# Optimization experiments

Hardware: AMD Instinct MI355X
Metric: run time of the kernel (lower is better)

Reference implementation:

```python
import jax, jax.numpy as jnp
import numpy as np

B, S, E, H = 2, 2048, 2048, 16
D = E // H  # head_dim = 128
EPS = 1e-5


def setup_inputs() -> dict:
    key = jax.random.key(0)
    ks = jax.random.split(key, 16)
    s_e = 1.0 / np.sqrt(E)
    s_f = 1.0 / np.sqrt(4 * E)
    return {
        "x": jax.random.normal(ks[0], (B, S, E), jnp.float32),
        "ln1_w": jnp.ones((E,), jnp.float32) + 0.01 * jax.random.normal(ks[1], (E,)),
        "ln1_b": 0.01 * jax.random.normal(ks[2], (E,)),
        "wq": s_e * jax.random.normal(ks[3], (E, E), jnp.float32),
        "wk": s_e * jax.random.normal(ks[4], (E, E), jnp.float32),
        "wv": s_e * jax.random.normal(ks[5], (E, E), jnp.float32),
        "wo": s_e * jax.random.normal(ks[6], (E, E), jnp.float32),
        "bo": 0.01 * jax.random.normal(ks[7], (E,)),
        "ln2_w": jnp.ones((E,), jnp.float32) + 0.01 * jax.random.normal(ks[8], (E,)),
        "ln2_b": 0.01 * jax.random.normal(ks[9], (E,)),
        "w1": s_e * jax.random.normal(ks[10], (E, 4 * E), jnp.float32),
        "b1": 0.01 * jax.random.normal(ks[11], (4 * E,)),
        "w2": s_f * jax.random.normal(ks[12], (4 * E, E), jnp.float32),
        "b2": 0.01 * jax.random.normal(ks[13], (E,)),
    }


def _layernorm(x, w, b):
    mu = jnp.mean(x, axis=-1, keepdims=True)
    var = jnp.var(x, axis=-1, keepdims=True)
    return (x - mu) * jax.lax.rsqrt(var + EPS) * w + b


def _attention(x, wq, wk, wv, wo, bo):
    # x: [B,S,E] -> q,k,v: [B,H,S,D]
    def split(t):
        return t.reshape(B, S, H, D).transpose(0, 2, 1, 3)
    q = split(x @ wq)
    k = split(x @ wk)
    v = split(x @ wv)
    scores = jnp.einsum("bhqd,bhkd->bhqk", q, k)  # [B,H,S,S]
    causal = jnp.triu(jnp.ones((S, S), bool), k=1)
    scores = jnp.where(causal, -jnp.inf, scores)
    # NOTE: faithful to source -- scaling applied after masking, inside softmax arg
    attn = jax.nn.softmax(scores / np.sqrt(D), axis=-1)
    ctx = jnp.einsum("bhqk,bhkd->bhqd", attn, v)
    ctx = ctx.transpose(0, 2, 1, 3).reshape(B, S, E)
    return ctx @ wo + bo


def reference(x, ln1_w, ln1_b, wq, wk, wv, wo, bo, ln2_w, ln2_b, w1, b1, w2, b2):
    shortcut = x
    x1 = _layernorm(x, ln1_w, ln1_b)
    attn_out = _attention(x1, wq, wk, wv, wo, bo)
    a = attn_out + shortcut
    # NOTE: faithful to source quirk -- second shortcut is post-LN1 x1, not a
    y = _layernorm(a, ln2_w, ln2_b)
    y = jax.nn.gelu(y @ w1 + b1, approximate=False) @ w2 + b2
    return x1 + y
```

## Files before the change

### kernel.cpp

```cpp
#include <hip/hip_runtime.h>
#include <math.h>

typedef unsigned short u16;
typedef unsigned int u32;
typedef __attribute__((ext_vector_type(8))) short short8;
typedef __attribute__((ext_vector_type(4))) float f32x4;
typedef __attribute__((ext_vector_type(16))) float f32x16;
typedef __attribute__((ext_vector_type(4))) u32 u32x4;
typedef __attribute__((ext_vector_type(2))) u32 u32x2;

#define DEVFN static __device__ __forceinline__

DEVFN u16 f2bf(float x) {
  union { float f; u32 u; } v; v.f = x;
  u32 r = v.u + 0x7fffu + ((v.u >> 16) & 1u);
  return (u16)(r >> 16);
}
DEVFN float bf2f(u16 h) {
  union { u32 u; float f; } v; v.u = ((u32)h) << 16;
  return v.f;
}
DEVFN u32 packbf2(float a, float b) {
  return (u32)f2bf(a) | ((u32)f2bf(b) << 16);
}
DEVFN void gl2lds16(const u16* g, u16* l) {
  __builtin_amdgcn_global_load_lds(
      (const __attribute__((address_space(1))) u32*)g,
      (__attribute__((address_space(3))) u32*)l, 16, 0, 0);
}
DEVFN float gelu_exact(float v) {
  float s = v * 0.70710678118654752f;
  float ax = fabsf(s);
  float t = __builtin_amdgcn_rcpf(1.0f + 0.3275911f * ax);
  float poly = t * (0.254829592f +
               t * (-0.284496736f +
               t * (1.421413741f +
               t * (-1.453152027f + t * 1.061405429f))));
  float e = __expf(-s * s);
  float er = 1.0f - poly * e;
  er = (s < 0.f) ? -er : er;
  return 0.5f * v * (1.0f + er);
}

#define VMW8() asm volatile("s_waitcnt vmcnt(8)" ::: "memory")
#define VMW6() asm volatile("s_waitcnt vmcnt(6)" ::: "memory")
#define VMW2() asm volatile("s_waitcnt vmcnt(2)" ::: "memory")
#define VMW0() asm volatile("s_waitcnt vmcnt(0)" ::: "memory")
#define LGKM0() asm volatile("s_waitcnt lgkmcnt(0)" ::: "memory")
#define CFENCE() asm volatile("" ::: "memory")
#define BARRIER() do { CFENCE(); __builtin_amdgcn_s_barrier(); CFENCE(); } while (0)

__global__ __launch_bounds__(256) void tconv_k(const float* __restrict__ in,
                                               u16* __restrict__ out, int K, int N) {
  __shared__ float tile[32][33];
  int n0 = blockIdx.x << 5, k0 = blockIdx.y << 5;
  int tx = threadIdx.x & 31, ty = threadIdx.x >> 5;
#pragma unroll
  for (int i = 0; i < 32; i += 8)
    tile[ty + i][tx] = in[(long)(k0 + ty + i) * N + n0 + tx];
  __syncthreads();
#pragma unroll
  for (int i = 0; i < 32; i += 8)
    out[(long)(n0 + ty + i) * K + k0 + tx] = f2bf(tile[tx][ty + i]);
}

__global__ __launch_bounds__(256) void ln1_k(const float* __restrict__ x,
                                             const float* __restrict__ w,
                                             const float* __restrict__ b,
                                             float* __restrict__ y32,
                                             u16* __restrict__ y16) {
  long base = (long)blockIdx.x * 2048;
  int t = threadIdx.x;
  float4 v0 = ((const float4*)(x + base))[2 * t];
  float4 v1 = ((const float4*)(x + base))[2 * t + 1];
  float xv[8];
  *(float4*)xv = v0; *(float4*)(xv + 4) = v1;
  float s = 0.f, ss = 0.f;
#pragma unroll
  for (int i = 0; i < 8; ++i) { s += xv[i]; ss += xv[i] * xv[i]; }
#pragma unroll
  for (int m = 1; m < 64; m <<= 1) { s += __shfl_xor(s, m); ss += __shfl_xor(ss, m); }
  __shared__ float rs[4], rss[4];
  int wave = t >> 6;
  if ((t & 63) == 0) { rs[wave] = s; rss[wave] = ss; }
  __syncthreads();
  s = rs[0] + rs[1] + rs[2] + rs[3];
  ss = rss[0] + rss[1] + rss[2] + rss[3];
  float mean = s * (1.f / 2048.f);
  float var = ss * (1.f / 2048.f) - mean * mean;
  float inv = rsqrtf(var + 1e-5f);
  float wv[8], bv[8];
  *(float4*)wv = ((const float4*)w)[2 * t]; *(float4*)(wv + 4) = ((const float4*)w)[2 * t + 1];
  *(float4*)bv = ((const float4*)b)[2 * t]; *(float4*)(bv + 4) = ((const float4*)b)[2 * t + 1];
  float yv[8];
#pragma unroll
  for (int i = 0; i < 8; ++i) yv[i] = (xv[i] - mean) * inv * wv[i] + bv[i];
  ((float4*)(y32 + base))[2 * t] = *(float4*)yv;
  ((float4*)(y32 + base))[2 * t + 1] = *(float4*)(yv + 4);
  u32x4 ov;
#pragma unroll
  for (int i = 0; i < 4; ++i) ov[i] = packbf2(yv[2 * i], yv[2 * i + 1]);
  ((u32x4*)(y16 + base))[t] = ov;
}

__global__ __launch_bounds__(256) void ln2_k(const u16* __restrict__ a,
                                             const float* __restrict__ w,
                                             const float* __restrict__ b,
                                             u16* __restrict__ y) {
  long base = (long)blockIdx.x * 2048;
  int t = threadIdx.x;
  u32x4 pv = ((const u32x4*)(a + base))[t];
  float xv[8];
#pragma unroll
  for (int i = 0; i < 4; ++i) {
    xv[2 * i] = bf2f((u16)(pv[i] & 0xffffu));
    xv[2 * i + 1] = bf2f((u16)(pv[i] >> 16));
  }
  float s = 0.f, ss = 0.f;
#pragma unroll
  for (int i = 0; i < 8; ++i) { s += xv[i]; ss += xv[i] * xv[i]; }
#pragma unroll
  for (int m = 1; m < 64; m <<= 1) { s += __shfl_xor(s, m); ss += __shfl_xor(ss, m); }
  __shared__ float rs[4], rss[4];
  int wave = t >> 6;
  if ((t & 63) == 0) { rs[wave] = s; rss[wave] = ss; }
  __syncthreads();
  s = rs[0] + rs[1] + rs[2] + rs[3];
  ss = rss[0] + rss[1] + rss[2] + rss[3];
  float mean = s * (1.f / 2048.f);
  float var = ss * (1.f / 2048.f) - mean * mean;
  float inv = rsqrtf(var + 1e-5f);
  float wv[8], bv[8];
  *(float4*)wv = ((const float4*)w)[2 * t]; *(float4*)(wv + 4) = ((const float4*)w)[2 * t + 1];
  *(float4*)bv = ((const float4*)b)[2 * t]; *(float4*)(bv + 4) = ((const float4*)b)[2 * t + 1];
  u32x4 ov;
#pragma unroll
  for (int i = 0; i < 4; ++i) {
    float y0 = (xv[2 * i] - mean) * inv * wv[2 * i] + bv[2 * i];
    float y1 = (xv[2 * i + 1] - mean) * inv * wv[2 * i + 1] + bv[2 * i + 1];
    ov[i] = packbf2(y0, y1);
  }
  ((u32x4*)(y + base))[t] = ov;
}

template <int MODE>
__global__ __launch_bounds__(512, 2) void gemm2x_k(const u16* __restrict__ A,
                                                   const u16* __restrict__ W,
                                                   void* __restrict__ outp,
                                                   const float* __restrict__ bias) {
  constexpr int nM = 16;
  constexpr int nN = (MODE == 0) ? 24 : (MODE == 3) ? 32 : 8;
  constexpr int KS = (MODE == 5) ? 2 : 1;
  constexpr int KK = (MODE == 5) ? 4096 : 2048;
  constexpr long LD = (MODE == 5) ? 8192 : 2048;
  constexpr int nt = KK / 64;
  constexpr int nwg = nM * nN * KS;
  __shared__ __align__(16) u16 lds[2][32768];
  const int t = threadIdx.x, lane = t & 63, wave = t >> 6;
  const int g = lane >> 4, r16 = lane & 15;
  const int wm = wave >> 2, wn = wave & 3;
  const int orig = blockIdx.y * gridDim.x + blockIdx.x;
  const int sw = (orig & 7) * (nwg >> 3) + (orig >> 3);
  const int mi = sw % nM;
  const int rest = sw / nM;
  const int ni = (MODE == 5) ? (rest & 7) : rest;
  const int ks = (MODE == 5) ? (rest >> 3) : 0;
  const long m0 = (long)mi * 256, n0 = (long)ni * 256;
  const long k0 = (long)ks * 4096;
  const int rl = lane >> 3, cl = lane & 7;

  auto stA = [&](int b, int half, int tile) {
#pragma unroll
    for (int q = 0; q < 2; ++q) {
      int rr = (wave * 2 + q) * 8 + rl;
      gl2lds16(A + (m0 + half * 128 + rr) * LD + k0 + (long)tile * 64 + (cl ^ (rr & 7)) * 8,
               &lds[b][half * 8192 + (wave * 2 + q) * 512]);
    }
  };
  auto stB = [&](int b, int half, int tile) {
#pragma unroll
    for (int q = 0; q < 2; ++q) {
      int rr = (wave * 2 + q) * 8 + rl;
      gl2lds16(W + (n0 + half * 128 + rr) * LD + k0 + (long)tile * 64 + (cl ^ (rr & 7)) * 8,
               &lds[b][16384 + half * 8192 + (wave * 2 + q) * 512]);
    }
  };

  f32x4 acc[8][4] = {};
  stA(0, 0, 0); stA(0, 1, 0); stB(0, 0, 0); stB(0, 1, 0);
  stA(1, 0, 1); stA(1, 1, 1); stB(1, 0, 1); stB(1, 1, 1);

  for (int tt = 0; tt < nt; ++tt) {
    const int cur = tt & 1;
    const u16* Lc = &lds[cur][0];
    VMW8();
    BARRIER();
    short8 a0[8], b0[4];
#pragma unroll
    for (int ii = 0; ii < 8; ++ii) {
      int row = wm * 128 + ii * 16 + r16;
      a0[ii] = *(const short8*)(Lc + row * 64 + (g ^ (row & 7)) * 8);
    }
#pragma unroll
    for (int jj = 0; jj < 4; ++jj) {
      int row = wn * 64 + jj * 16 + r16;
      b0[jj] = *(const short8*)(Lc + 16384 + row * 64 + (g ^ (row & 7)) * 8);
    }
    __builtin_amdgcn_s_setprio(1);
#pragma unroll
    for (int ii = 0; ii < 8; ++ii)
#pragma unroll
      for (int jj = 0; jj < 4; ++jj)
        acc[ii][jj] = __builtin_amdgcn_mfma_f32_16x16x32_bf16(a0[ii], b0[jj], acc[ii][jj], 0, 0, 0);
    __builtin_amdgcn_s_setprio(0);
    short8 a1[8], b1f[4];
#pragma unroll
    for (int ii = 0; ii < 8; ++ii) {
      int row = wm * 128 + ii * 16 + r16;
      a1[ii] = *(const short8*)(Lc + row * 64 + ((4 | g) ^ (row & 7)) * 8);
    }
#pragma unroll
    for (int jj = 0; jj < 4; ++jj) {
      int row = wn * 64 + jj * 16 + r16;
      b1f[jj] = *(const short8*)(Lc + 16384 + row * 64 + ((4 | g) ^ (row & 7)) * 8);
    }
    LGKM0();
    BARRIER();
    {
      const int ts = (tt + 2 < nt) ? tt + 2 : nt - 1;
      stA(cur, 0, ts); stA(cur, 1, ts); stB(cur, 0, ts); stB(cur, 1, ts);
    }
    __builtin_amdgcn_s_setprio(1);
#pragma unroll
    for (int ii = 0; ii < 8; ++ii)
#pragma unroll
      for (int jj = 0; jj < 4; ++jj)
        acc[ii][jj] = __builtin_amdgcn_mfma_f32_16x16x32_bf16(a1[ii], b1f[jj], acc[ii][jj], 0, 0, 0);
    __builtin_amdgcn_s_setprio(0);
  }
  VMW0();

#pragma unroll
  for (int ii = 0; ii < 8; ++ii) {
#pragma unroll
    for (int jj = 0; jj < 4; ++jj) {
#pragma unroll
      for (int r = 0; r < 4; ++r) {
        long mg = m0 + wm * 128 + ii * 16 + g * 4 + r;
        long ng = n0 + wn * 64 + jj * 16 + r16;
        float v = acc[ii][jj][r];
        if constexpr (MODE == 0) {
          long which = ng >> 11;
          long nloc = ng & 2047;
          long bb = mg >> 11, sq = mg & 2047;
          long hh = nloc >> 7, dd = nloc & 127;
          long idx = (which < 2) ? (((bb * 16 + hh) * 2048 + sq) * 128 + dd)
                                 : (((bb * 16 + hh) * 128 + dd) * 2048 + sq);
          ((u16*)outp)[which * 8388608 + idx] = f2bf(v);
        } else if constexpr (MODE == 3) {
          v = gelu_exact(v + bias[ng]);
          ((u16*)outp)[mg * 8192 + ng] = f2bf(v);
        } else {
          ((float*)outp)[(long)ks * 8388608 + mg * 2048 + ng] = v;
        }
      }
    }
  }
}

__global__ __launch_bounds__(256) void red_k(const float* __restrict__ p,
                                             const float* __restrict__ bias,
                                             const float* __restrict__ resid,
                                             float* __restrict__ out) {
  long i = (long)blockIdx.x * 256 + threadIdx.x;
  for (long idx = i; idx < 2097152; idx += 2048 * 256) {
    float4 a = ((const float4*)p)[idx];
    float4 b = ((const float4*)(p + 8388608))[idx];
    float4 r = ((const float4*)resid)[idx];
    float4 bs = ((const float4*)bias)[idx & 511];
    float4 o;
    o.x = a.x + b.x + r.x + bs.x;
    o.y = a.y + b.y + r.y + bs.y;
    o.z = a.z + b.z + r.z + bs.z;
    o.w = a.w + b.w + r.w + bs.w;
    ((float4*)out)[idx] = o;
  }
}

template <int MODE>
__global__ __launch_bounds__(512, 2) void gemm3_k(const u16* __restrict__ A,
                                                  const u16* __restrict__ W,
                                                  void* __restrict__ outp,
                                                  const float* __restrict__ bias,
                                                  const float* __restrict__ resid,
                                                  int M, int N, int K) {
  __shared__ __align__(16) u16 lds[3][24576];
  const int t = threadIdx.x, lane = t & 63, wave = t >> 6;
  const int g = lane >> 4, r16 = lane & 15;
  const int wm = wave >> 2, wn = wave & 3;
  const int nM = M >> 7;
  const int nwg = gridDim.x * gridDim.y;
  const int orig = blockIdx.y * gridDim.x + blockIdx.x;
  const int sw = (nwg & 7) ? orig : ((orig & 7) * (nwg >> 3) + (orig >> 3));
  const long m0 = (long)(sw % nM) * 128, n0 = (long)(sw / nM) * 256;
  const int nt = K >> 6;
  const long Kl = K;
  const int rl = lane >> 3, cc = lane & 7;

  auto stA = [&](u16* Lb, long tile) {
#pragma unroll
    for (int q = 0; q < 2; ++q) {
      int rr = (wave * 2 + q) * 8 + rl;
      int c = cc ^ (rr & 7);
      gl2lds16(A + (m0 + rr) * Kl + (tile << 6) + c * 8, Lb + (wave * 2 + q) * 512);
    }
  };
  auto stB = [&](u16* Lb, int half, long tile) {
#pragma unroll
    for (int q = 0; q < 2; ++q) {
      int rr = (wave * 2 + q) * 8 + rl;
      int c = cc ^ (rr & 7);
      gl2lds16(W + (n0 + half * 128 + rr) * Kl + (tile << 6) + c * 8,
               Lb + 8192 + half * 8192 + (wave * 2 + q) * 512);
    }
  };

  f32x4 acc[4][4] = {};
  u16* L0 = &lds[0][0];
  u16* L1 = &lds[1][0];
  u16* L2 = &lds[2][0];

  stA(L0, 0); stB(L0, 0, 0); stB(L0, 1, 0);
  if (nt > 1) { stA(L1, 1); stB(L1, 0, 1); stB(L1, 1, 1); }
  if (nt > 2) { VMW6(); } else { VMW0(); }
  BARRIER();

  for (int tt = 0; tt < nt; ++tt) {
    const long ts = (tt + 2 < nt) ? (long)(tt + 2) : (long)(nt - 1);
    short8 af[4][2], bf[2][2];
#pragma unroll
    for (int ii2 = 0; ii2 < 4; ++ii2) {
      int row = (ii2 * 2 + wm) * 16 + r16;
#pragma unroll
      for (int kk = 0; kk < 2; ++kk)
        af[ii2][kk] = *(const short8*)(L0 + row * 64 + (((kk << 2) | g) ^ (row & 7)) * 8);
    }
#pragma unroll
    for (int jj2 = 0; jj2 < 2; ++jj2) {
      int row = (jj2 * 4 + wn) * 16 + r16;
#pragma unroll
      for (int kk = 0; kk < 2; ++kk)
        bf[jj2][kk] = *(const short8*)(L0 + 8192 + row * 64 + (((kk << 2) | g) ^ (row & 7)) * 8);
    }
    stA(L2, ts); stB(L2, 0, ts);
    __builtin_amdgcn_s_setprio(1);
#pragma unroll
    for (int ii2 = 0; ii2 < 4; ++ii2)
#pragma unroll
      for (int jj2 = 0; jj2 < 2; ++jj2)
#pragma unroll
        for (int kk = 0; kk < 2; ++kk)
          acc[ii2][jj2] = __builtin_amdgcn_mfma_f32_16x16x32_bf16(
              af[ii2][kk], bf[jj2][kk], acc[ii2][jj2], 0, 0, 0);
    __builtin_amdgcn_s_setprio(0);
    BARRIER();
#pragma unroll
    for (int jj2 = 0; jj2 < 2; ++jj2) {
      int row = ((2 + jj2) * 4 + wn) * 16 + r16;
#pragma unroll
      for (int kk = 0; kk < 2; ++kk)
        bf[jj2][kk] = *(const short8*)(L0 + 8192 + row * 64 + (((kk << 2) | g) ^ (row & 7)) * 8);
    }
    stB(L2, 1, ts);
    __builtin_amdgcn_s_setprio(1);
#pragma unroll
    for (int ii2 = 0; ii2 < 4; ++ii2)
#pragma unroll
      for (int jj2 = 0; jj2 < 2; ++jj2)
#pragma unroll
        for (int kk = 0; kk < 2; ++kk)
          acc[ii2][2 + jj2] = __builtin_amdgcn_mfma_f32_16x16x32_bf16(
              af[ii2][kk], bf[jj2][kk], acc[ii2][2 + jj2], 0, 0, 0);
    __builtin_amdgcn_s_setprio(0);
    VMW6(); BARRIER();
    u16* tmp = L0; L0 = L1; L1 = L2; L2 = tmp;
  }
  VMW0();

  const long Nl = N;
#pragma unroll
  for (int ii = 0; ii < 4; ++ii) {
#pragma unroll
    for (int jj = 0; jj < 4; ++jj) {
#pragma unroll
      for (int r = 0; r < 4; ++r) {
        long mg = m0 + (ii * 2 + wm) * 16 + g * 4 + r;
        long ng = n0 + (jj * 4 + wn) * 16 + r16;
        float v = acc[ii][jj][r];
        if constexpr (MODE == 2) {
          v += bias[ng] + resid[mg * Nl + ng];
          ((u16*)outp)[mg * Nl + ng] = f2bf(v);
        } else {
          v += bias[ng] + resid[mg * Nl + ng];
          ((float*)outp)[mg * Nl + ng] = v;
        }
      }
    }
  }
}

__global__ __launch_bounds__(256, 2) void attn2_k(const u16* __restrict__ Qp,
                                                  const u16* __restrict__ Kp,
                                                  const u16* __restrict__ Vp,
                                                  u16* __restrict__ ctx) {
  __shared__ __align__(16) u16 KsL[2][64 * 128];
  __shared__ __align__(16) u16 VsL[2][128 * 64];
  const int qt = gridDim.x - 1 - blockIdx.x;
  const int bh = blockIdx.y;
  const int t = threadIdx.x, lane = t & 63, wave = t >> 6;
  const int l31 = lane & 31, hi = lane >> 5;
  const int q0 = qt * 128, qw0 = q0 + wave * 32;
  const int qg = qw0 + l31;
  const u16* Qh = Qp + (long)bh * 2048 * 128;
  const u16* Kh = Kp + (long)bh * 2048 * 128;
  const u16* Vh = Vp + (long)bh * 128 * 2048;
  const int nkt = qt * 2 + 2;
  const int ktmax = (qw0 + 31) >> 6;
  const float cs = 0.12753042923810058f;

  short8 qf[8];
#pragma unroll
  for (int ds = 0; ds < 8; ++ds)
    qf[ds] = *(const short8*)(Qh + (long)qg * 128 + ds * 16 + hi * 8);

  f32x16 O0 = {}, O1 = {}, O2 = {}, O3 = {};
  float m = -INFINITY, l = 0.f;

  auto stage = [&](int b, int kt) {
#pragma unroll
    for (int q = 0; q < 4; ++q) {
      int r = wave * 16 + q * 4 + (lane >> 4);
      int c = (lane & 15) ^ (r & 15);
      gl2lds16(Kh + ((long)kt * 64 + r) * 128 + c * 8,
               &KsL[b][(wave * 16 + q * 4) * 128]);
    }
#pragma unroll
    for (int q = 0; q < 4; ++q) {
      int r = wave * 32 + q * 8 + (lane >> 3);
      int c = (lane & 7) ^ (r & 7);
      gl2lds16(Vh + (long)r * 2048 + kt * 64 + c * 8,
               &VsL[b][(wave * 32 + q * 8) * 64]);
    }
  };

  stage(0, 0);
  VMW0(); BARRIER();

  for (int kt = 0; kt < nkt; ++kt) {
    const int cur = kt & 1;
    if (kt + 1 < nkt) stage(cur ^ 1, kt + 1);
    if (kt <= ktmax) {
      f32x16 S0 = {}, S1 = {};
      __builtin_amdgcn_s_setprio(1);
#pragma unroll
      for (int ds = 0; ds < 8; ++ds) {
        int c0 = ((ds * 2 + hi) ^ (l31 & 15)) * 8;
        short8 k0 = *(const short8*)(&KsL[cur][l31 * 128 + c0]);
        int r1 = 32 + l31;
        int c1 = ((ds * 2 + hi) ^ (r1 & 15)) * 8;
        short8 k1 = *(const short8*)(&KsL[cur][r1 * 128 + c1]);
        S0 = __builtin_amdgcn_mfma_f32_32x32x16_bf16(k0, qf[ds], S0, 0, 0, 0);
        S1 = __builtin_amdgcn_mfma_f32_32x32x16_bf16(k1, qf[ds], S1, 0, 0, 0);
      }
      __builtin_amdgcn_s_setprio(0);
      float p[32];
#pragma unroll
      for (int i = 0; i < 16; ++i) { p[i] = S0[i]; p[16 + i] = S1[i]; }
      if (kt * 64 + 63 > qw0) {
#pragma unroll
        for (int ks = 0; ks < 2; ++ks)
#pragma unroll
          for (int r = 0; r < 16; ++r) {
            int kg = kt * 64 + ks * 32 + (r & 3) + 8 * (r >> 2) + 4 * hi;
            if (kg > qg) p[ks * 16 + r] = -INFINITY;
          }
      }
      float tmax = p[0];
#pragma unroll
      for (int i = 1; i < 32; ++i) tmax = fmaxf(tmax, p[i]);
      tmax = fmaxf(tmax, __shfl_xor(tmax, 32));
      float mnew = fmaxf(m, tmax);
      float corr = __builtin_amdgcn_exp2f((m - mnew) * cs);
      float ls = 0.f;
#pragma unroll
      for (int i = 0; i < 32; ++i) {
        p[i] = __builtin_amdgcn_exp2f((p[i] - mnew) * cs);
        ls += p[i];
      }
      ls += __shfl_xor(ls, 32);
      l = l * corr + ls;
      m = mnew;
#pragma unroll
      for (int i = 0; i < 16; ++i) {
        O0[i] *= corr; O1[i] *= corr; O2[i] *= corr; O3[i] *= corr;
      }
      short8 pf[4];
#pragma unroll
      for (int gg = 0; gg < 4; ++gg) {
        u32 u_, v_, w_, z_;
        asm("v_cvt_pk_bf16_f32 %0, %1, %2" : "=v"(u_) : "v"(p[gg * 8 + 0]), "v"(p[gg * 8 + 1]));
        asm("v_cvt_pk_bf16_f32 %0, %1, %2" : "=v"(v_) : "v"(p[gg * 8 + 2]), "v"(p[gg * 8 + 3]));
        asm("v_cvt_pk_bf16_f32 %0, %1, %2" : "=v"(w_) : "v"(p[gg * 8 + 4]), "v"(p[gg * 8 + 5]));
        asm("v_cvt_pk_bf16_f32 %0, %1, %2" : "=v"(z_) : "v"(p[gg * 8 + 6]), "v"(p[gg * 8 + 7]));
        asm("v_permlane32_swap_b32 %0, %1" : "+v"(u_), "+v"(w_));
        asm("v_permlane32_swap_b32 %0, %1" : "+v"(v_), "+v"(z_));
        union { u32 w4[4]; short8 s; } cv;
        cv.w4[0] = u_; cv.w4[1] = v_; cv.w4[2] = w_; cv.w4[3] = z_;
        pf[gg] = cv.s;
      }
      __builtin_amdgcn_s_setprio(1);
#define PVROW(ds, OO)                                                          \
  {                                                                            \
    int row = (ds)*32 + l31;                                                   \
    _Pragma("unroll") for (int gg = 0; gg < 4; ++gg) {                         \
      short8 vf = *(const short8*)(&VsL[cur][row * 64 +                        \
                                             (((gg * 2 + hi) ^ (row & 7)) * 8)]); \
      OO = __builtin_amdgcn_mfma_f32_32x32x16_bf16(vf, pf[gg], OO, 0, 0, 0);   \
    }                                                                          \
  }
      PVROW(0, O0); PVROW(1, O1); PVROW(2, O2); PVROW(3, O3);
#undef PVROW
      __builtin_amdgcn_s_setprio(0);
    }
    VMW0(); BARRIER();
  }

  const float inv = 1.f / l;
  u16* cp = ctx + ((long)(bh >> 4) * 2048 + qg) * 2048 + (bh & 15) * 128;
#define WROUT(OO, dsb)                                                         \
  _Pragma("unroll") for (int rg = 0; rg < 4; ++rg) {                           \
    int d = (dsb)*32 + 8 * rg + 4 * hi;                                        \
    u32x2 wv;                                                                  \
    wv[0] = packbf2(OO[4 * rg] * inv, OO[4 * rg + 1] * inv);                   \
    wv[1] = packbf2(OO[4 * rg + 2] * inv, OO[4 * rg + 3] * inv);               \
    *(u32x2*)(cp + d) = wv;                                                    \
  }
  WROUT(O0, 0); WROUT(O1, 1); WROUT(O2, 2); WROUT(O3, 3);
#undef WROUT
}

extern "C" void kernel_launch(void* const* d_in, const int* in_sizes, int n_in,
                              void* d_out, int out_size, void* d_ws, size_t ws_size,
                              hipStream_t stream) {
  const float* x = (const float*)d_in[0];
  const float* ln1w = (const float*)d_in[1];
  const float* ln1b = (const float*)d_in[2];
  const float* wq = (const float*)d_in[3];
  const float* wk = (const float*)d_in[4];
  const float* wv = (const float*)d_in[5];
  const float* wo = (const float*)d_in[6];
  const float* bo = (const float*)d_in[7];
  const float* ln2w = (const float*)d_in[8];
  const float* ln2b = (const float*)d_in[9];
  const float* w1 = (const float*)d_in[10];
  const float* b1 = (const float*)d_in[11];
  const float* w2 = (const float*)d_in[12];
  const float* b2 = (const float*)d_in[13];
  float* out = (float*)d_out;
  char* ws = (char*)d_ws;

  float* x1f = (float*)(ws + 0);
  u16* x1b = (u16*)(ws + 33554432);
  u16* wqt = (u16*)(ws + 50331648);
  u16* wkt = (u16*)(ws + 58720256);
  u16* wvt = (u16*)(ws + 67108864);
  u16* wot = (u16*)(ws + 75497472);
  u16* w1t = (u16*)(ws + 83886080);
  u16* w2t = (u16*)(ws + 117440512);
  u16* qb = (u16*)(ws + 150994944);
  u16* kb = (u16*)(ws + 167772160);
  u16* vb = (u16*)(ws + 184549376);
  u16* ctxb = (u16*)(ws + 201326592);
  u16* ab = (u16*)(ws + 218103808);
  u16* y0b = (u16*)(ws + 234881024);
  u16* hb = qb;
  float* pbuf = (float*)(ws + 50331648);

  tconv_k<<<dim3(64, 64), 256, 0, stream>>>(wq, wqt, 2048, 2048);
  tconv_k<<<dim3(64, 64), 256, 0, stream>>>(wk, wkt, 2048, 2048);
  tconv_k<<<dim3(64, 64), 256, 0, stream>>>(wv, wvt, 2048, 2048);
  tconv_k<<<dim3(64, 64), 256, 0, stream>>>(wo, wot, 2048, 2048);
  tconv_k<<<dim3(256, 64), 256, 0, stream>>>(w1, w1t, 2048, 8192);
  tconv_k<<<dim3(64, 256), 256, 0, stream>>>(w2, w2t, 8192, 2048);
  ln1_k<<<4096, 256, 0, stream>>>(x, ln1w, ln1b, x1f, x1b);
  gemm2x_k<0><<<dim3(16, 24), 512, 0, stream>>>(x1b, wqt, qb, nullptr);
  attn2_k<<<dim3(16, 32), 256, 0, stream>>>(qb, kb, vb, ctxb);
  gemm3_k<2><<<dim3(32, 8), 512, 0, stream>>>(ctxb, wot, ab, bo, x, 4096, 2048, 2048);
  ln2_k<<<4096, 256, 0, stream>>>(ab, ln2w, ln2b, y0b);
  gemm2x_k<3><<<dim3(16, 32), 512, 0, stream>>>(y0b, w1t, hb, b1);
  gemm2x_k<5><<<dim3(16, 16), 512, 0, stream>>>(hb, w2t, pbuf, nullptr);
  red_k<<<2048, 256, 0, stream>>>(pbuf, b2, x1f, out);
}
```

Measured before the change: 644.0 us.

## Restructure big GEMM main loop into four-phase quadrant ping-pong schedule

The 256x256 GEMM main loop is reorganised into four quadrant phases (A-low/B-low, A-low/B-high, A-high/B-low, A-high/B-high). Each phase uses both k-halves, and the global-to-LDS loads for the next tile are spread between the phases with barriers in between. The LDS staging layout is rearranged so each quarter-tile can be refilled once its readers are finished. The goal is to interleave LDS reads, global prefetch and MFMA work more finely, in the style of an 8-wave ping-pong. Launch bounds drop to one block per CU, and the extra barriers add synchronisation cost.

```diff
diff --git a/kernel.cpp b/kernel.cpp
--- a/kernel.cpp
+++ b/kernel.cpp
@@ -44,7 +44,6 @@
 
 #define VMW8() asm volatile("s_waitcnt vmcnt(8)" ::: "memory")
 #define VMW6() asm volatile("s_waitcnt vmcnt(6)" ::: "memory")
-#define VMW2() asm volatile("s_waitcnt vmcnt(2)" ::: "memory")
 #define VMW0() asm volatile("s_waitcnt vmcnt(0)" ::: "memory")
 #define LGKM0() asm volatile("s_waitcnt lgkmcnt(0)" ::: "memory")
 #define CFENCE() asm volatile("" ::: "memory")
@@ -144,7 +143,7 @@
 }
 
 template <int MODE>
-__global__ __launch_bounds__(512, 2) void gemm2x_k(const u16* __restrict__ A,
+__global__ __launch_bounds__(512, 1) void gemm8p_k(const u16* __restrict__ A,
                                                    const u16* __restrict__ W,
                                                    void* __restrict__ outp,
                                                    const float* __restrict__ bias) {
@@ -169,74 +168,116 @@
   const long k0 = (long)ks * 4096;
   const int rl = lane >> 3, cl = lane & 7;
 
-  auto stA = [&](int b, int half, int tile) {
+  auto stAq = [&](int b, int grp, int ts) {
 #pragma unroll
     for (int q = 0; q < 2; ++q) {
-      int rr = (wave * 2 + q) * 8 + rl;
-      gl2lds16(A + (m0 + half * 128 + rr) * LD + k0 + (long)tile * 64 + (cl ^ (rr & 7)) * 8,
-               &lds[b][half * 8192 + (wave * 2 + q) * 512]);
+      int rb = q * 128 + grp * 64 + wave * 8;
+      int rr = rb + rl;
+      gl2lds16(A + (m0 + rr) * LD + k0 + (long)ts * 64 + (cl ^ (rr & 7)) * 8,
+               &lds[b][rb * 64]);
     }
   };
-  auto stB = [&](int b, int half, int tile) {
+  auto stBq = [&](int b, int grp, int ts) {
 #pragma unroll
     for (int q = 0; q < 2; ++q) {
-      int rr = (wave * 2 + q) * 8 + rl;
-      gl2lds16(W + (n0 + half * 128 + rr) * LD + k0 + (long)tile * 64 + (cl ^ (rr & 7)) * 8,
-               &lds[b][16384 + half * 8192 + (wave * 2 + q) * 512]);
+      int rb = q * 128 + (wave >> 2) * 64 + (wave & 3) * 8 + grp * 32;
+      int rr = rb + rl;
+      gl2lds16(W + (n0 + rr) * LD + k0 + (long)ts * 64 + (cl ^ (rr & 7)) * 8,
+               &lds[b][16384 + rb * 64]);
     }
   };
 
   f32x4 acc[8][4] = {};
-  stA(0, 0, 0); stA(0, 1, 0); stB(0, 0, 0); stB(0, 1, 0);
-  stA(1, 0, 1); stA(1, 1, 1); stB(1, 0, 1); stB(1, 1, 1);
+  short8 afl[4][2], afh[4][2], bfl[2][2], bfh[2][2];
+
+  stAq(0, 0, 0); stBq(0, 0, 0); stAq(0, 1, 0); stBq(0, 1, 0);
+  stAq(1, 0, 1); stBq(1, 0, 1); stAq(1, 1, 1); stBq(1, 1, 1);
+  VMW8();
+  BARRIER();
 
   for (int tt = 0; tt < nt; ++tt) {
     const int cur = tt & 1;
     const u16* Lc = &lds[cur][0];
-    VMW8();
+    const int ts = (tt + 2 < nt) ? tt + 2 : nt - 1;
+#pragma unroll
+    for (int ii = 0; ii < 4; ++ii) {
+      int row = wm * 128 + ii * 16 + r16;
+#pragma unroll
+      for (int kk = 0; kk < 2; ++kk)
+        afl[ii][kk] = *(const short8*)(Lc + row * 64 + (((kk << 2) | g) ^ (row & 7)) * 8);
+    }
+#pragma unroll
+    for (int jj = 0; jj < 2; ++jj) {
+      int row = wn * 64 + jj * 16 + r16;
+#pragma unroll
+      for (int kk = 0; kk < 2; ++kk)
+        bfl[jj][kk] = *(const short8*)(Lc + 16384 + row * 64 + (((kk << 2) | g) ^ (row & 7)) * 8);
+    }
+    BARRIER(); LGKM0();
+    __builtin_amdgcn_s_setprio(1);
+#pragma unroll
+    for (int ii = 0; ii < 4; ++ii)
+#pragma unroll
+      for (int jj = 0; jj < 2; ++jj)
+#pragma unroll
+        for (int kk = 0; kk < 2; ++kk)
+          acc[ii][jj] = __builtin_amdgcn_mfma_f32_16x16x32_bf16(
+              afl[ii][kk], bfl[jj][kk], acc[ii][jj], 0, 0, 0);
+    __builtin_amdgcn_s_setprio(0);
     BARRIER();
-    short8 a0[8], b0[4];
-#pragma unroll
-    for (int ii = 0; ii < 8; ++ii) {
-      int row = wm * 128 + ii * 16 + r16;
-      a0[ii] = *(const short8*)(Lc + row * 64 + (g ^ (row & 7)) * 8);
-    }
-#pragma unroll
-    for (int jj = 0; jj < 4; ++jj) {
-      int row = wn * 64 + jj * 16 + r16;
-      b0[jj] = *(const short8*)(Lc + 16384 + row * 64 + (g ^ (row & 7)) * 8);
-    }
+#pragma unroll
+    for (int jj = 0; jj < 2; ++jj) {
+      int row = wn * 64 + 32 + jj * 16 + r16;
+#pragma unroll
+      for (int kk = 0; kk < 2; ++kk)
+        bfh[jj][kk] = *(const short8*)(Lc + 16384 + row * 64 + (((kk << 2) | g) ^ (row & 7)) * 8);
+    }
+    stAq(cur, 0, ts);
+    BARRIER(); LGKM0();
     __builtin_amdgcn_s_setprio(1);
 #pragma unroll
-    for (int ii = 0; ii < 8; ++ii)
-#pragma unroll
-      for (int jj = 0; jj < 4; ++jj)
-        acc[ii][jj] = __builtin_amdgcn_mfma_f32_16x16x32_bf16(a0[ii], b0[jj], acc[ii][jj], 0, 0, 0);
+    for (int ii = 0; ii < 4; ++ii)
+#pragma unroll
+      for (int jj = 0; jj < 2; ++jj)
+#pragma unroll
+        for (int kk = 0; kk < 2; ++kk)
+          acc[ii][2 + jj] = __builtin_amdgcn_mfma_f32_16x16x32_bf16(
+              afl[ii][kk], bfh[jj][kk], acc[ii][2 + jj], 0, 0, 0);
     __builtin_amdgcn_s_setprio(0);
-    short8 a1[8], b1f[4];
-#pragma unroll
-    for (int ii = 0; ii < 8; ++ii) {
-      int row = wm * 128 + ii * 16 + r16;
-      a1[ii] = *(const short8*)(Lc + row * 64 + ((4 | g) ^ (row & 7)) * 8);
-    }
-#pragma unroll
-    for (int jj = 0; jj < 4; ++jj) {
-      int row = wn * 64 + jj * 16 + r16;
-      b1f[jj] = *(const short8*)(Lc + 16384 + row * 64 + ((4 | g) ^ (row & 7)) * 8);
-    }
-    LGKM0();
     BARRIER();
-    {
-      const int ts = (tt + 2 < nt) ? tt + 2 : nt - 1;
-      stA(cur, 0, ts); stA(cur, 1, ts); stB(cur, 0, ts); stB(cur, 1, ts);
-    }
+#pragma unroll
+    for (int ii = 0; ii < 4; ++ii) {
+      int row = wm * 128 + 64 + ii * 16 + r16;
+#pragma unroll
+      for (int kk = 0; kk < 2; ++kk)
+        afh[ii][kk] = *(const short8*)(Lc + row * 64 + (((kk << 2) | g) ^ (row & 7)) * 8);
+    }
+    stBq(cur, 0, ts);
+    BARRIER(); LGKM0();
     __builtin_amdgcn_s_setprio(1);
 #pragma unroll
-    for (int ii = 0; ii < 8; ++ii)
-#pragma unroll
-      for (int jj = 0; jj < 4; ++jj)
-        acc[ii][jj] = __builtin_amdgcn_mfma_f32_16x16x32_bf16(a1[ii], b1f[jj], acc[ii][jj], 0, 0, 0);
+    for (int ii = 0; ii < 4; ++ii)
+#pragma unroll
+      for (int jj = 0; jj < 2; ++jj)
+#pragma unroll
+        for (int kk = 0; kk < 2; ++kk)
+          acc[4 + ii][jj] = __builtin_amdgcn_mfma_f32_16x16x32_bf16(
+              afh[ii][kk], bfl[jj][kk], acc[4 + ii][jj], 0, 0, 0);
     __builtin_amdgcn_s_setprio(0);
+    BARRIER();
+    stAq(cur, 1, ts); stBq(cur, 1, ts);
+    __builtin_amdgcn_s_setprio(1);
+#pragma unroll
+    for (int ii = 0; ii < 4; ++ii)
+#pragma unroll
+      for (int jj = 0; jj < 2; ++jj)
+#pragma unroll
+        for (int kk = 0; kk < 2; ++kk)
+          acc[4 + ii][2 + jj] = __builtin_amdgcn_mfma_f32_16x16x32_bf16(
+              afh[ii][kk], bfh[jj][kk], acc[4 + ii][2 + jj], 0, 0, 0);
+    __builtin_amdgcn_s_setprio(0);
+    VMW6();
+    BARRIER();
   }
   VMW0();
 
@@ -397,11 +438,10 @@
         long mg = m0 + (ii * 2 + wm) * 16 + g * 4 + r;
         long ng = n0 + (jj * 4 + wn) * 16 + r16;
         float v = acc[ii][jj][r];
+        v += bias[ng] + resid[mg * Nl + ng];
         if constexpr (MODE == 2) {
-          v += bias[ng] + resid[mg * Nl + ng];
           ((u16*)outp)[mg * Nl + ng] = f2bf(v);
         } else {
-          v += bias[ng] + resid[mg * Nl + ng];
           ((float*)outp)[mg * Nl + ng] = v;
         }
       }
@@ -593,11 +633,11 @@
   tconv_k<<<dim3(256, 64), 256, 0, stream>>>(w1, w1t, 2048, 8192);
   tconv_k<<<dim3(64, 256), 256, 0, stream>>>(w2, w2t, 8192, 2048);
   ln1_k<<<4096, 256, 0, stream>>>(x, ln1w, ln1b, x1f, x1b);
-  gemm2x_k<0><<<dim3(16, 24), 512, 0, stream>>>(x1b, wqt, qb, nullptr);
+  gemm8p_k<0><<<dim3(16, 24), 512, 0, stream>>>(x1b, wqt, qb, nullptr);
   attn2_k<<<dim3(16, 32), 256, 0, stream>>>(qb, kb, vb, ctxb);
   gemm3_k<2><<<dim3(32, 8), 512, 0, stream>>>(ctxb, wot, ab, bo, x, 4096, 2048, 2048);
   ln2_k<<<4096, 256, 0, stream>>>(ab, ln2w, ln2b, y0b);
-  gemm2x_k<3><<<dim3(16, 32), 512, 0, stream>>>(y0b, w1t, hb, b1);
-  gemm2x_k<5><<<dim3(16, 16), 512, 0, stream>>>(hb, w2t, pbuf, nullptr);
+  gemm8p_k<3><<<dim3(16, 32), 512, 0, stream>>>(y0b, w1t, hb, b1);
+  gemm8p_k<5><<<dim3(16, 16), 512, 0, stream>>>(hb, w2t, pbuf, nullptr);
   red_k<<<2048, 256, 0, stream>>>(pbuf, b2, x1f, out);
 }
```

After: 643.8 us. About the same (-0.0%).
